# Performance work log

Hardware: AMD Instinct MI355X
Metric: run time of the kernel (lower is better)

The kernel has to match this reference:

```python
import jax, jax.numpy as jnp
import numpy as np

FEATURE_DIM = 128
N_NODES = 100000
N_EDGES = 800000
L1_IN = 2 * FEATURE_DIM            # 256
L1_OUT = int((2 * FEATURE_DIM) ** 0.5)  # 16
L2_DIM = L1_OUT + 1                # 17


def leaky(x):
    return jnp.where(x >= 0, x, 0.1 * x)


def setup_inputs() -> dict:
    key = jax.random.key(0)
    ks = jax.random.split(key, 8)
    Jt_ind = jax.random.randint(ks[0], (2, N_EDGES), 0, N_NODES)
    Jt_val = jax.random.normal(ks[1], (N_EDGES,), dtype=jnp.float32)
    f = jax.random.normal(ks[2], (N_NODES, FEATURE_DIM), dtype=jnp.float32)
    W1 = jax.random.normal(ks[3], (L1_IN, L1_OUT), dtype=jnp.float32) * (1.0 / np.sqrt(L1_IN))
    b1 = jnp.zeros((L1_OUT,), dtype=jnp.float32)
    W2 = jax.random.normal(ks[4], (L2_DIM, L2_DIM), dtype=jnp.float32) * (1.0 / np.sqrt(L2_DIM))
    b2 = jnp.zeros((L2_DIM,), dtype=jnp.float32)
    Wc = jax.random.normal(ks[5], (L2_DIM, 1), dtype=jnp.float32) * (1.0 / np.sqrt(L2_DIM))
    bc = jnp.ones((1,), dtype=jnp.float32)  # collapse_bias = 1
    return {"Jt_ind": Jt_ind, "Jt_val": Jt_val, "f": f, "N": N_NODES,
            "W1": W1, "b1": b1, "W2": W2, "b2": b2, "Wc": Wc, "bc": bc}


def reference(Jt_ind, Jt_val, f, N, W1, b1, W2, b2, Wc, bc):
    i = Jt_ind[0]
    j = Jt_ind[1]
    absv = jnp.abs(Jt_val)                                     # [E]
    # degree: per-destination sum of |Jt_val|
    deg_abs = jax.ops.segment_sum(absv, i, num_segments=N)     # [N]
    Jt_val_abs_norm = absv / deg_abs[i]                        # [E]
    # gather endpoint features and run tiny edge-MLP
    x = jnp.concatenate([f[i], f[j]], axis=1)                  # [E, 2F]
    x = leaky(x @ W1 + b1)                                     # [E, L1_OUT]
    x = jnp.concatenate([x, Jt_val_abs_norm[:, None]], axis=1) # [E, L2_DIM]
    x = leaky(x @ W2 + b2)                                     # [E, L2_DIM]
    e_values = (x @ Wc + bc)[:, 0]                             # [E]
    # segment softmax over edges grouped by destination i (stable)
    m = jax.ops.segment_max(e_values, i, num_segments=N)       # [N]
    ex = jnp.exp(e_values - m[i])                              # [E]
    s = jax.ops.segment_sum(ex, i, num_segments=N)             # [N]
    return ex / s[i]                                           # [E]
```

## Files before the change

### kernel.cpp

```cpp
#include <hip/hip_runtime.h>
#include <hip/hip_fp16.h>
#include <math.h>

#define FDIM  128
#define L1OUT 16
#define L2DIM 17

struct H16 { __half2 h[8]; };

__device__ __forceinline__ float lrelu(float v) { return v >= 0.f ? v : 0.1f * v; }

__global__ void init_nodes(float* __restrict__ deg, float* __restrict__ ssum, int N) {
    int n = blockIdx.x * blockDim.x + threadIdx.x;
    if (n < N) { deg[n] = 0.f; ssum[n] = 0.f; }
}

__global__ void node_transform(const float* __restrict__ f,
                               const float* __restrict__ W1,
                               H16* __restrict__ A, H16* __restrict__ B, int N) {
    int n = blockIdx.x * blockDim.x + threadIdx.x;
    if (n >= N) return;
    const float4* frow = reinterpret_cast<const float4*>(f + (size_t)n * FDIM);
    float accA[L1OUT], accB[L1OUT];
#pragma unroll
    for (int c = 0; c < L1OUT; ++c) { accA[c] = 0.f; accB[c] = 0.f; }

    for (int k4 = 0; k4 < FDIM / 4; ++k4) {
        float4 fv = frow[k4];
        const float* wA = W1 + (size_t)(k4 * 4) * L1OUT;
        const float* wB = W1 + (size_t)(FDIM + k4 * 4) * L1OUT;
#pragma unroll
        for (int c = 0; c < L1OUT; ++c) {
            accA[c] += fv.x * wA[0 * L1OUT + c];
            accA[c] += fv.y * wA[1 * L1OUT + c];
            accA[c] += fv.z * wA[2 * L1OUT + c];
            accA[c] += fv.w * wA[3 * L1OUT + c];
            accB[c] += fv.x * wB[0 * L1OUT + c];
            accB[c] += fv.y * wB[1 * L1OUT + c];
            accB[c] += fv.z * wB[2 * L1OUT + c];
            accB[c] += fv.w * wB[3 * L1OUT + c];
        }
    }
    H16 pa, pb;
#pragma unroll
    for (int q = 0; q < 8; ++q) {
        pa.h[q] = __floats2half2_rn(accA[2 * q], accA[2 * q + 1]);
        pb.h[q] = __floats2half2_rn(accB[2 * q], accB[2 * q + 1]);
    }
    A[n] = pa;
    B[n] = pb;
}

__global__ void deg_accum(const int* __restrict__ ind_i, const float* __restrict__ val,
                          float* __restrict__ deg, int E) {
    int t = blockIdx.x * blockDim.x + threadIdx.x;
    int e = t * 4;
    if (e + 3 < E) {
        int4   ii = *reinterpret_cast<const int4*>(ind_i + e);
        float4 vv = *reinterpret_cast<const float4*>(val + e);
        atomicAdd(&deg[ii.x], fabsf(vv.x));
        atomicAdd(&deg[ii.y], fabsf(vv.y));
        atomicAdd(&deg[ii.z], fabsf(vv.z));
        atomicAdd(&deg[ii.w], fabsf(vv.w));
    } else {
        for (; e < E; ++e) atomicAdd(&deg[ind_i[e]], fabsf(val[e]));
    }
}

__device__ __forceinline__ float edge_val(const H16& a, const H16& b, float nv,
                                          const float* __restrict__ b1,
                                          const float* __restrict__ W2,
                                          const float* __restrict__ b2,
                                          const float* __restrict__ Wc, float bc0) {
    float x[L2DIM];
#pragma unroll
    for (int q = 0; q < 8; ++q) {
        float2 fa = __half22float2(a.h[q]);
        float2 fb = __half22float2(b.h[q]);
        x[2 * q]     = lrelu(fa.x + fb.x + b1[2 * q]);
        x[2 * q + 1] = lrelu(fa.y + fb.y + b1[2 * q + 1]);
    }
    x[L1OUT] = nv;
    float ev = bc0;
#pragma unroll
    for (int r = 0; r < L2DIM; ++r) {
        float acc = b2[r];
#pragma unroll
        for (int c = 0; c < L2DIM; ++c) acc += x[c] * W2[c * L2DIM + r];
        ev += lrelu(acc) * Wc[r];
    }
    return ev;
}

__global__ void edge_mlp(const int* __restrict__ ind, const float* __restrict__ val,
                         const H16* __restrict__ A, const H16* __restrict__ B,
                         const float* __restrict__ deg,
                         const float* __restrict__ b1,
                         const float* __restrict__ W2, const float* __restrict__ b2,
                         const float* __restrict__ Wc, const float* __restrict__ bc,
                         float* __restrict__ eout, float* __restrict__ ssum,
                         int E, int Eh) {
    int t = blockIdx.x * blockDim.x + threadIdx.x;
    if (t >= Eh) return;
    int e0 = t, e1 = t + Eh;
    bool has1 = (e1 < E);

    int i0 = ind[e0], j0 = ind[E + e0];
    int i1 = has1 ? ind[e1] : i0;
    int j1 = has1 ? ind[E + e1] : j0;

    H16 a0 = A[i0], bb0 = B[j0];
    H16 a1 = A[i1], bb1 = B[j1];

    float nv0 = fabsf(val[e0]) / deg[i0];
    float nv1 = has1 ? (fabsf(val[e1]) / deg[i1]) : 0.f;

    float bc0 = bc[0];
    float ev0 = edge_val(a0, bb0, nv0, b1, W2, b2, Wc, bc0);
    float ex0 = __expf(ev0);
    eout[e0] = ex0;
    atomicAdd(&ssum[i0], ex0);

    if (has1) {
        float ev1 = edge_val(a1, bb1, nv1, b1, W2, b2, Wc, bc0);
        float ex1 = __expf(ev1);
        eout[e1] = ex1;
        atomicAdd(&ssum[i1], ex1);
    }
}

__global__ void normalize(const int* __restrict__ ind_i, const float* __restrict__ ssum,
                          float* __restrict__ ex, int E, int Eh) {
    int t = blockIdx.x * blockDim.x + threadIdx.x;
    if (t >= Eh) return;
    int e0 = t, e1 = t + Eh;
    int i0 = ind_i[e0];
    float v0 = ex[e0];
    if (e1 < E) {
        int i1 = ind_i[e1];
        float v1 = ex[e1];
        ex[e1] = v1 / ssum[i1];
    }
    ex[e0] = v0 / ssum[i0];
}

extern "C" void kernel_launch(void* const* d_in, const int* in_sizes, int n_in,
                              void* d_out, int out_size, void* d_ws, size_t ws_size,
                              hipStream_t stream) {
    const int*   Jt_ind = (const int*)  d_in[0];
    const float* Jt_val = (const float*)d_in[1];
    const float* f      = (const float*)d_in[2];
    const float* W1 = (const float*)d_in[4];
    const float* b1 = (const float*)d_in[5];
    const float* W2 = (const float*)d_in[6];
    const float* b2 = (const float*)d_in[7];
    const float* Wc = (const float*)d_in[8];
    const float* bc = (const float*)d_in[9];

    const int E  = in_sizes[1];
    const int N  = in_sizes[2] / FDIM;
    const int Eh = (E + 1) / 2;
    float* out = (float*)d_out;

    char* ws = (char*)d_ws;
    H16*   A    = (H16*)ws;    ws += (size_t)N * sizeof(H16);
    H16*   Bm   = (H16*)ws;    ws += (size_t)N * sizeof(H16);
    float* deg  = (float*)ws;  ws += (size_t)N * sizeof(float);
    float* ssum = (float*)ws;  ws += (size_t)N * sizeof(float);

    const int B256 = 256;
    init_nodes    <<<(N + B256 - 1) / B256, B256, 0, stream>>>(deg, ssum, N);
    node_transform<<<(N + B256 - 1) / B256, B256, 0, stream>>>(f, W1, A, Bm, N);
    deg_accum     <<<(E / 4 + B256 - 1) / B256 + 1, B256, 0, stream>>>(Jt_ind, Jt_val, deg, E);
    edge_mlp      <<<(Eh + B256 - 1) / B256, B256, 0, stream>>>(Jt_ind, Jt_val, A, Bm, deg,
                                                                b1, W2, b2, Wc, bc,
                                                                out, ssum, E, Eh);
    normalize     <<<(Eh + B256 - 1) / B256, B256, 0, stream>>>(Jt_ind, ssum, out, E, Eh);
}
```

Measured before the change: 237.7 us.

## Tile node transform through shared memory and simplify edge and normalize kernels

The node transform now stages a 64-row tile of features and all of W1 in shared memory. Four waves each compute 8 output columns for one half of K, which replaces the per-thread strided row reads with coalesced loads. Zeroing of deg and ssum is folded into this kernel, so the separate init launch goes away. The edge MLP now processes one edge per thread with W2, biases and Wc cached in shared memory and read as float4, and normalize handles four edges per thread with vector loads. The cost is more shared memory per block, which can lower occupancy, plus extra per-block weight-staging work in the edge kernel.

Result: faster. 232.9 us (-2.0%).

```diff
diff --git a/kernel.cpp b/kernel.cpp
--- a/kernel.cpp
+++ b/kernel.cpp
@@ -5,50 +5,78 @@
 #define FDIM  128
 #define L1OUT 16
 #define L2DIM 17
-
-struct H16 { __half2 h[8]; };
+#define TR    64
+#define TSTR  129
+
+struct __align__(16) H16 { __half2 h[8]; };
 
 __device__ __forceinline__ float lrelu(float v) { return v >= 0.f ? v : 0.1f * v; }
-
-__global__ void init_nodes(float* __restrict__ deg, float* __restrict__ ssum, int N) {
-    int n = blockIdx.x * blockDim.x + threadIdx.x;
-    if (n < N) { deg[n] = 0.f; ssum[n] = 0.f; }
-}
 
 __global__ void node_transform(const float* __restrict__ f,
                                const float* __restrict__ W1,
-                               H16* __restrict__ A, H16* __restrict__ B, int N) {
-    int n = blockIdx.x * blockDim.x + threadIdx.x;
-    if (n >= N) return;
-    const float4* frow = reinterpret_cast<const float4*>(f + (size_t)n * FDIM);
-    float accA[L1OUT], accB[L1OUT];
-#pragma unroll
-    for (int c = 0; c < L1OUT; ++c) { accA[c] = 0.f; accB[c] = 0.f; }
-
-    for (int k4 = 0; k4 < FDIM / 4; ++k4) {
-        float4 fv = frow[k4];
-        const float* wA = W1 + (size_t)(k4 * 4) * L1OUT;
-        const float* wB = W1 + (size_t)(FDIM + k4 * 4) * L1OUT;
-#pragma unroll
-        for (int c = 0; c < L1OUT; ++c) {
-            accA[c] += fv.x * wA[0 * L1OUT + c];
-            accA[c] += fv.y * wA[1 * L1OUT + c];
-            accA[c] += fv.z * wA[2 * L1OUT + c];
-            accA[c] += fv.w * wA[3 * L1OUT + c];
-            accB[c] += fv.x * wB[0 * L1OUT + c];
-            accB[c] += fv.y * wB[1 * L1OUT + c];
-            accB[c] += fv.z * wB[2 * L1OUT + c];
-            accB[c] += fv.w * wB[3 * L1OUT + c];
-        }
-    }
-    H16 pa, pb;
+                               H16* __restrict__ A, H16* __restrict__ B,
+                               float* __restrict__ deg, float* __restrict__ ssum,
+                               int N) {
+    __shared__ float tile[TR * TSTR];
+    __shared__ float w1s[256 * L1OUT];
+
+    int t   = threadIdx.x;
+    int gid = blockIdx.x * 256 + t;
+    if (gid < N) { deg[gid] = 0.f; ssum[gid] = 0.f; }
+
+    {
+        const float4* src = reinterpret_cast<const float4*>(W1);
+        float4*       dst = reinterpret_cast<float4*>(w1s);
+#pragma unroll
+        for (int q = 0; q < 4; ++q) dst[t + 256 * q] = src[t + 256 * q];
+    }
+    int base = blockIdx.x * TR;
 #pragma unroll
     for (int q = 0; q < 8; ++q) {
-        pa.h[q] = __floats2half2_rn(accA[2 * q], accA[2 * q + 1]);
-        pb.h[q] = __floats2half2_rn(accB[2 * q], accB[2 * q + 1]);
-    }
-    A[n] = pa;
-    B[n] = pb;
+        int i4 = t + 256 * q;
+        int r  = i4 >> 5;
+        int c4 = i4 & 31;
+        float4 v = make_float4(0.f, 0.f, 0.f, 0.f);
+        if (base + r < N)
+            v = reinterpret_cast<const float4*>(f + (size_t)(base + r) * FDIM)[c4];
+        float* d = &tile[r * TSTR + c4 * 4];
+        d[0] = v.x; d[1] = v.y; d[2] = v.z; d[3] = v.w;
+    }
+    __syncthreads();
+
+    int lane    = t & 63;
+    int w       = t >> 6;
+    int colbase = (w & 1) * 8;
+    int krowoff = (w >> 1) * FDIM;
+
+    float acc[8];
+#pragma unroll
+    for (int c = 0; c < 8; ++c) acc[c] = 0.f;
+
+    const float* trow  = &tile[lane * TSTR];
+    const float* wbase = &w1s[krowoff * L1OUT + colbase];
+#pragma unroll 4
+    for (int k = 0; k < FDIM; ++k) {
+        float x = trow[k];
+        const float4* wr = reinterpret_cast<const float4*>(wbase + k * L1OUT);
+        float4 w0 = wr[0], w1v = wr[1];
+        acc[0] += x * w0.x;  acc[1] += x * w0.y;
+        acc[2] += x * w0.z;  acc[3] += x * w0.w;
+        acc[4] += x * w1v.x; acc[5] += x * w1v.y;
+        acc[6] += x * w1v.z; acc[7] += x * w1v.w;
+    }
+
+    int n = base + lane;
+    if (n < N) {
+        __half2 h[4];
+#pragma unroll
+        for (int q = 0; q < 4; ++q)
+            h[q] = __floats2half2_rn(acc[2 * q], acc[2 * q + 1]);
+        H16* arr = (w >> 1) ? B : A;
+        float4* dst = reinterpret_cast<float4*>(
+            reinterpret_cast<char*>(arr + n) + (w & 1) * 16);
+        *dst = *reinterpret_cast<float4*>(h);
+    }
 }
 
 __global__ void deg_accum(const int* __restrict__ ind_i, const float* __restrict__ val,
@@ -67,81 +95,93 @@
     }
 }
 
-__device__ __forceinline__ float edge_val(const H16& a, const H16& b, float nv,
-                                          const float* __restrict__ b1,
-                                          const float* __restrict__ W2,
-                                          const float* __restrict__ b2,
-                                          const float* __restrict__ Wc, float bc0) {
-    float x[L2DIM];
-#pragma unroll
-    for (int q = 0; q < 8; ++q) {
-        float2 fa = __half22float2(a.h[q]);
-        float2 fb = __half22float2(b.h[q]);
-        x[2 * q]     = lrelu(fa.x + fb.x + b1[2 * q]);
-        x[2 * q + 1] = lrelu(fa.y + fb.y + b1[2 * q + 1]);
-    }
-    x[L1OUT] = nv;
-    float ev = bc0;
-#pragma unroll
-    for (int r = 0; r < L2DIM; ++r) {
-        float acc = b2[r];
-#pragma unroll
-        for (int c = 0; c < L2DIM; ++c) acc += x[c] * W2[c * L2DIM + r];
-        ev += lrelu(acc) * Wc[r];
-    }
-    return ev;
-}
-
 __global__ void edge_mlp(const int* __restrict__ ind, const float* __restrict__ val,
                          const H16* __restrict__ A, const H16* __restrict__ B,
                          const float* __restrict__ deg,
                          const float* __restrict__ b1,
                          const float* __restrict__ W2, const float* __restrict__ b2,
                          const float* __restrict__ Wc, const float* __restrict__ bc,
-                         float* __restrict__ eout, float* __restrict__ ssum,
-                         int E, int Eh) {
+                         float* __restrict__ eout, float* __restrict__ ssum, int E) {
+    __shared__ float w2s[L2DIM * 20];
+    __shared__ float b1s[L1OUT];
+    __shared__ float b2s[L2DIM];
+    __shared__ float wcs[L2DIM];
+    __shared__ float bc0s;
+
+    int t = threadIdx.x;
+    for (int idx = t; idx < L2DIM * L2DIM; idx += 256) {
+        int c = idx / L2DIM, r = idx % L2DIM;
+        w2s[c * 20 + r] = W2[idx];
+    }
+    if (t < L1OUT) b1s[t] = b1[t];
+    if (t < L2DIM) b2s[t] = b2[t];
+    if (t < L2DIM) wcs[t] = Wc[t];
+    if (t == 0)    bc0s   = bc[0];
+    __syncthreads();
+
+    int e = blockIdx.x * 256 + t;
+    if (e >= E) return;
+
+    int i = ind[e];
+    int j = ind[E + e];
+    H16 a  = A[i];
+    H16 bb = B[j];
+    float v  = val[e];
+    float dg = deg[i];
+
+    float x[L2DIM];
+#pragma unroll
+    for (int q = 0; q < 8; ++q) {
+        float2 fa = __half22float2(a.h[q]);
+        float2 fb = __half22float2(bb.h[q]);
+        x[2 * q]     = lrelu(fa.x + fb.x + b1s[2 * q]);
+        x[2 * q + 1] = lrelu(fa.y + fb.y + b1s[2 * q + 1]);
+    }
+    x[L1OUT] = fabsf(v) / dg;
+
+    float acc[L2DIM];
+#pragma unroll
+    for (int r = 0; r < L2DIM; ++r) acc[r] = b2s[r];
+#pragma unroll
+    for (int c = 0; c < L2DIM; ++c) {
+        float xc = x[c];
+        const float4* r4 = reinterpret_cast<const float4*>(&w2s[c * 20]);
+        float4 w0 = r4[0], w1 = r4[1], w2v = r4[2], w3 = r4[3];
+        float  w16 = w2s[c * 20 + 16];
+        acc[0]  += xc * w0.x;  acc[1]  += xc * w0.y;
+        acc[2]  += xc * w0.z;  acc[3]  += xc * w0.w;
+        acc[4]  += xc * w1.x;  acc[5]  += xc * w1.y;
+        acc[6]  += xc * w1.z;  acc[7]  += xc * w1.w;
+        acc[8]  += xc * w2v.x; acc[9]  += xc * w2v.y;
+        acc[10] += xc * w2v.z; acc[11] += xc * w2v.w;
+        acc[12] += xc * w3.x;  acc[13] += xc * w3.y;
+        acc[14] += xc * w3.z;  acc[15] += xc * w3.w;
+        acc[16] += xc * w16;
+    }
+    float ev = bc0s;
+#pragma unroll
+    for (int r = 0; r < L2DIM; ++r) ev += lrelu(acc[r]) * wcs[r];
+
+    float ex = __expf(ev);
+    eout[e] = ex;
+    atomicAdd(&ssum[i], ex);
+}
+
+__global__ void normalize(const int* __restrict__ ind_i, const float* __restrict__ ssum,
+                          float* __restrict__ ex, int E) {
     int t = blockIdx.x * blockDim.x + threadIdx.x;
-    if (t >= Eh) return;
-    int e0 = t, e1 = t + Eh;
-    bool has1 = (e1 < E);
-
-    int i0 = ind[e0], j0 = ind[E + e0];
-    int i1 = has1 ? ind[e1] : i0;
-    int j1 = has1 ? ind[E + e1] : j0;
-
-    H16 a0 = A[i0], bb0 = B[j0];
-    H16 a1 = A[i1], bb1 = B[j1];
-
-    float nv0 = fabsf(val[e0]) / deg[i0];
-    float nv1 = has1 ? (fabsf(val[e1]) / deg[i1]) : 0.f;
-
-    float bc0 = bc[0];
-    float ev0 = edge_val(a0, bb0, nv0, b1, W2, b2, Wc, bc0);
-    float ex0 = __expf(ev0);
-    eout[e0] = ex0;
-    atomicAdd(&ssum[i0], ex0);
-
-    if (has1) {
-        float ev1 = edge_val(a1, bb1, nv1, b1, W2, b2, Wc, bc0);
-        float ex1 = __expf(ev1);
-        eout[e1] = ex1;
-        atomicAdd(&ssum[i1], ex1);
-    }
-}
-
-__global__ void normalize(const int* __restrict__ ind_i, const float* __restrict__ ssum,
-                          float* __restrict__ ex, int E, int Eh) {
-    int t = blockIdx.x * blockDim.x + threadIdx.x;
-    if (t >= Eh) return;
-    int e0 = t, e1 = t + Eh;
-    int i0 = ind_i[e0];
-    float v0 = ex[e0];
-    if (e1 < E) {
-        int i1 = ind_i[e1];
-        float v1 = ex[e1];
-        ex[e1] = v1 / ssum[i1];
-    }
-    ex[e0] = v0 / ssum[i0];
+    int e = t * 4;
+    if (e + 3 < E) {
+        int4   ii = *reinterpret_cast<const int4*>(ind_i + e);
+        float4 vv = *reinterpret_cast<const float4*>(ex + e);
+        vv.x /= ssum[ii.x];
+        vv.y /= ssum[ii.y];
+        vv.z /= ssum[ii.z];
+        vv.w /= ssum[ii.w];
+        *reinterpret_cast<float4*>(ex + e) = vv;
+    } else {
+        for (; e < E; ++e) ex[e] = ex[e] / ssum[ind_i[e]];
+    }
 }
 
 extern "C" void kernel_launch(void* const* d_in, const int* in_sizes, int n_in,
@@ -157,9 +197,8 @@
     const float* Wc = (const float*)d_in[8];
     const float* bc = (const float*)d_in[9];
 
-    const int E  = in_sizes[1];
-    const int N  = in_sizes[2] / FDIM;
-    const int Eh = (E + 1) / 2;
+    const int E = in_sizes[1];
+    const int N = in_sizes[2] / FDIM;
     float* out = (float*)d_out;
 
     char* ws = (char*)d_ws;
@@ -169,11 +208,13 @@
     float* ssum = (float*)ws;  ws += (size_t)N * sizeof(float);
 
     const int B256 = 256;
-    init_nodes    <<<(N + B256 - 1) / B256, B256, 0, stream>>>(deg, ssum, N);
-    node_transform<<<(N + B256 - 1) / B256, B256, 0, stream>>>(f, W1, A, Bm, N);
-    deg_accum     <<<(E / 4 + B256 - 1) / B256 + 1, B256, 0, stream>>>(Jt_ind, Jt_val, deg, E);
-    edge_mlp      <<<(Eh + B256 - 1) / B256, B256, 0, stream>>>(Jt_ind, Jt_val, A, Bm, deg,
-                                                                b1, W2, b2, Wc, bc,
-                                                                out, ssum, E, Eh);
-    normalize     <<<(Eh + B256 - 1) / B256, B256, 0, stream>>>(Jt_ind, ssum, out, E, Eh);
-}
+    const int nblk = (N + TR - 1) / TR;
+    const int eblk = (E + B256 - 1) / B256;
+    const int qblk = ((E + 3) / 4 + B256 - 1) / B256;
+
+    node_transform<<<nblk, B256, 0, stream>>>(f, W1, A, Bm, deg, ssum, N);
+    deg_accum     <<<qblk, B256, 0, stream>>>(Jt_ind, Jt_val, deg, E);
+    edge_mlp      <<<eblk, B256, 0, stream>>>(Jt_ind, Jt_val, A, Bm, deg,
+                                              b1, W2, b2, Wc, bc, out, ssum, E);
+    normalize     <<<qblk, B256, 0, stream>>>(Jt_ind, ssum, out, E);
+}
```
